# Optimization experiments

Hardware: AMD Instinct MI355X
Metric: run time of the kernel (lower is better)

## Reference

```python
import jax, jax.numpy as jnp
import numpy as np

D = 768  # inputdim = k_size = v_size (forced equal by residual + LayerNorm)
B, T = 16, 2048


def setup_inputs() -> dict:
    key = jax.random.key(0)
    ks = jax.random.split(key, 9)
    s = 1.0 / np.sqrt(D)
    return {
        "x": jax.random.normal(ks[0], (B, T, D), dtype=jnp.float32),
        "Wk": jax.random.normal(ks[1], (D, D), dtype=jnp.float32) * s,
        "bk": jnp.zeros((D,), dtype=jnp.float32),
        "Wq": jax.random.normal(ks[2], (D, D), dtype=jnp.float32) * s,
        "bq": jnp.zeros((D,), dtype=jnp.float32),
        "Wv": jax.random.normal(ks[3], (D, D), dtype=jnp.float32) * s,
        "bv": jnp.zeros((D,), dtype=jnp.float32),
        "gamma": jnp.ones((D,), dtype=jnp.float32),
        "beta": jnp.zeros((D,), dtype=jnp.float32),
    }


def reference(x, Wk, bk, Wq, bq, Wv, bv, gamma, beta):
    sq_k = jnp.sqrt(jnp.asarray(D, dtype=x.dtype))
    keys = jnp.einsum("btd,kd->btk", x, Wk) + bk      # [B,T,K]
    queries = jnp.einsum("btd,kd->btk", x, Wq) + bq   # [B,T,K]
    values = jnp.einsum("btd,vd->btv", x, Wv) + bv    # [B,T,V]
    logits = jnp.einsum("bqk,btk->bqt", queries, keys)  # [B,Tq,Tk]
    # NB: original softmaxes over dim=1 (the QUERY axis), then scales AFTER softmax
    q_k = jax.nn.softmax(logits, axis=1) / sq_k
    applied = jnp.einsum("bqt,btv->bqv", q_k, values)  # [B,T,V]
    y = applied + x
    mu = jnp.mean(y, axis=-1, keepdims=True)
    var = jnp.mean(jnp.square(y - mu), axis=-1, keepdims=True)
    return (y - mu) * jax.lax.rsqrt(var + 1e-5) * gamma + beta
```

## Files before the change

kernel.cpp:

```cpp
#include <hip/hip_runtime.h>
#include <hip/hip_fp16.h>

#define DD 768
#define BB 16
#define TT 2048
#define BT (BB*TT)
#define NQS 8
#define BST 76

using f16 = _Float16;
typedef __attribute__((ext_vector_type(8))) f16 half8;
typedef __attribute__((ext_vector_type(4))) f16 half4;
typedef __attribute__((ext_vector_type(4))) float f32x4;

#define GSWZ(r) ((((r) & 3)) ^ (((r) >> 2) & 3))

typedef const __attribute__((address_space(1))) unsigned int* gas1;
typedef __attribute__((address_space(3))) unsigned int* las3;
__device__ __forceinline__ void gload16(const void* g, void* l){
  __builtin_amdgcn_global_load_lds((gas1)g, (las3)l, 16, 0, 0);
}

__global__ __launch_bounds__(256)
void tofp16_kernel(const float* __restrict__ src, f16* __restrict__ dst, int n4){
  const int stride = gridDim.x * 256;
  for (int i = blockIdx.x*256 + threadIdx.x; i < n4; i += stride){
    float4 v = ((const float4*)src)[i];
    half4 h; h[0]=(f16)v.x; h[1]=(f16)v.y; h[2]=(f16)v.z; h[3]=(f16)v.w;
    ((half4*)dst)[i] = h;
  }
}

template<int OMODE>
__global__ __launch_bounds__(256, OMODE==2 ? 3 : 2)
void gemmk(const f16* __restrict__ A, int lda, long sA,
           const f16* __restrict__ B, int ldb, long sB,
           void* __restrict__ Out, int ldc, long sC,
           const float* __restrict__ aux, int Kdim,
           float* __restrict__ f0, float* __restrict__ f1,
           const f16* __restrict__ cs, f16* __restrict__ vt)
{
  constexpr int MR = (OMODE==2) ? 4 : 8;
  constexpr int BM = MR * 32;
  constexpr int AC = BM / 64;

  __shared__ f16 lA[3][BM*32];
  __shared__ f16 lB[3][128*32];
  __shared__ float smx[OMODE==1 ? 4 : 1][4][16], szx[OMODE==1 ? 4 : 1][4][16];
  __shared__ f16 lCC[OMODE==2 ? 2048 : 8];

  const int nx = gridDim.x, ny = gridDim.y, nwg = nx * ny, cpx = nwg >> 3;
  int h = blockIdx.x + nx * blockIdx.y;
  h = (h & 7) * cpx + (h >> 3);
  const int bx = h / ny, by = h % ny;

  const int b = blockIdx.z;
  const f16* A_ = A + (size_t)b * sA;
  const f16* B_ = B + (size_t)b * sB;
  const int m0 = bx * BM, n0 = by * 128;
  const int tid = threadIdx.x, lane = tid & 63, wave = tid >> 6;
  const int wm = wave >> 1, wn = wave & 1;

  size_t gaO[AC], gbO[2];
#pragma unroll
  for (int k = 0; k < AC; ++k){
    int c = k*256 + tid, r = c >> 2, s = (c & 3) ^ GSWZ(r);
    gaO[k] = (size_t)(m0 + r) * lda + s * 8;
  }
#pragma unroll
  for (int k = 0; k < 2; ++k){
    int c = k*256 + tid, r = c >> 2, s = (c & 3) ^ GSWZ(r);
    gbO[k] = (size_t)(n0 + r) * ldb + s * 8;
  }

  f32x4 acc[MR][4] = {};
  const int NT = Kdim >> 5;

  auto STAGE = [&](int u, int kt){
#pragma unroll
    for (int k = 0; k < AC; ++k) gload16(A_ + gaO[k] + kt, &lA[u][(k*256+tid)*8]);
#pragma unroll
    for (int k = 0; k < 2; ++k)  gload16(B_ + gbO[k] + kt, &lB[u][(k*256+tid)*8]);
  };

  if constexpr (OMODE == 2){
    const f16* cb = cs + ((size_t)b * NQS + (bx >> 1)) * TT;
    ((half8*)lCC)[tid] = ((const half8*)cb)[tid];
    __syncthreads();
  }

  STAGE(0, 0); STAGE(1, 32);

  const int frow = lane & 15;
  const int rsl = (((lane >> 4) ^ GSWZ(frow)) & 3) * 8;
  const int tsl = (lane >> 4) * 8;
  const int offA = (wm*(MR*16) + frow)*32 + rsl;
  const int offB = (wn*64 + frow)*32 + rsl;

  int u = 0;
  for (int t = 0; t < NT; ++t){
    int u2 = u + 2; if (u2 >= 3) u2 -= 3;
    __builtin_amdgcn_s_barrier();
    __builtin_amdgcn_sched_barrier(0);
    if (t + 2 < NT) STAGE(u2, (t + 2) * 32);
    const int rem = NT - 1 - t;
    if constexpr (AC == 4){
      if (rem >= 2)      asm volatile("s_waitcnt vmcnt(12)" ::: "memory");
      else if (rem == 1) asm volatile("s_waitcnt vmcnt(6)"  ::: "memory");
      else               asm volatile("s_waitcnt vmcnt(0)"  ::: "memory");
    } else {
      if (rem >= 2)      asm volatile("s_waitcnt vmcnt(8)" ::: "memory");
      else if (rem == 1) asm volatile("s_waitcnt vmcnt(4)" ::: "memory");
      else               asm volatile("s_waitcnt vmcnt(0)" ::: "memory");
    }
    __builtin_amdgcn_s_barrier();
    __builtin_amdgcn_sched_barrier(0);

    const f16* tA = &lA[u][0] + offA;
    const f16* tB = &lB[u][0] + offB;
    half8 af[MR], bf[4];
#pragma unroll
    for (int i = 0; i < MR; ++i) af[i] = *(const half8*)(tA + i*512);
#pragma unroll
    for (int j = 0; j < 4; ++j)  bf[j] = *(const half8*)(tB + j*512);
    if constexpr (OMODE == 2){
      half8 cc = *(const half8*)&lCC[t*32 + tsl];
#pragma unroll
      for (int i = 0; i < MR; ++i) af[i] *= cc;
    }
    __builtin_amdgcn_s_setprio(1);
#pragma unroll
    for (int i = 0; i < MR; ++i)
#pragma unroll
      for (int j = 0; j < 4; ++j)
        acc[i][j] = __builtin_amdgcn_mfma_f32_16x16x32_f16(af[i], bf[j], acc[i][j], 0,0,0);
    __builtin_amdgcn_s_setprio(0);
    u = (u + 1 == 3) ? 0 : u + 1;
  }

  __syncthreads();
  const int kq4 = (lane >> 4) * 4;
  f16* bnc = &lA[0][0] + wave * (16*BST);
  const int rrow = lane >> 2, rcol = (lane & 3) * 16;

  if constexpr (OMODE == 0 || OMODE == 2){
    const bool toVt = (OMODE == 0) && (b == 2);
    float bias4[4] = {};
    if constexpr (OMODE == 0){
#pragma unroll
      for (int j = 0; j < 4; ++j) bias4[j] = aux[b*DD + n0 + wn*64 + j*16 + frow];
    }
    f16* O = (OMODE == 0) ? ((f16*)Out + (size_t)b * sC) : ((f16*)Out + (size_t)b * sC);
#pragma unroll
    for (int i = 0; i < MR; ++i){
#pragma unroll
      for (int j = 0; j < 4; ++j)
#pragma unroll
        for (int r = 0; r < 4; ++r)
          bnc[(kq4 + r)*BST + j*16 + frow] = (f16)(acc[i][j][r] + bias4[j]);
      if (!toVt){
        half8 w0 = *(const half8*)&bnc[rrow*BST + rcol];
        half8 w1 = *(const half8*)&bnc[rrow*BST + rcol + 8];
        const int gr = m0 + wm*(MR*16) + i*16 + rrow;
        const int gc = n0 + wn*64 + rcol;
        *(half8*)&O[(size_t)gr*ldc + gc]     = w0;
        *(half8*)&O[(size_t)gr*ldc + gc + 8] = w1;
      } else {
        f16 tmp[16];
#pragma unroll
        for (int k = 0; k < 16; ++k) tmp[k] = bnc[k*BST + lane];
        half8 v0, v1;
#pragma unroll
        for (int k = 0; k < 8; ++k){ v0[k] = tmp[k]; v1[k] = tmp[8+k]; }
        const int tokg = m0 + wm*(MR*16) + i*16;
        const int batch = tokg >> 11, tok = tokg & (TT-1);
        f16* Vo = vt + ((size_t)batch*DD + n0 + wn*64 + lane)*TT + tok;
        *(half8*)&Vo[0] = v0;
        *(half8*)&Vo[8] = v1;
      }
    }
  } else {
    f16* O = (f16*)Out + (size_t)b * sC;
    float Mb[4];
#pragma unroll
    for (int j = 0; j < 4; ++j){
      float mx = acc[0][j][0];
#pragma unroll
      for (int i = 0; i < MR; ++i)
#pragma unroll
        for (int r = 0; r < 4; ++r) mx = fmaxf(mx, acc[i][j][r]);
      mx = fmaxf(mx, __shfl_xor(mx, 16, 64));
      mx = fmaxf(mx, __shfl_xor(mx, 32, 64));
      if (lane < 16) smx[wave][j][lane] = mx;
      Mb[j] = mx;
    }
    __syncthreads();
#pragma unroll
    for (int j = 0; j < 4; ++j)
      Mb[j] = fmaxf(Mb[j], smx[wave ^ 2][j][frow]);
    float zz[4] = {};
#pragma unroll
    for (int i = 0; i < MR; ++i){
#pragma unroll
      for (int j = 0; j < 4; ++j)
#pragma unroll
        for (int r = 0; r < 4; ++r){
          float e = __expf(acc[i][j][r] - Mb[j]);
          zz[j] += e;
          bnc[(kq4 + r)*BST + j*16 + frow] = (f16)e;
        }
      half8 w0 = *(const half8*)&bnc[rrow*BST + rcol];
      half8 w1 = *(const half8*)&bnc[rrow*BST + rcol + 8];
      const int gr = m0 + wm*(MR*16) + i*16 + rrow;
      const int gc = n0 + wn*64 + rcol;
      *(half8*)&O[(size_t)gr*ldc + gc]     = w0;
      *(half8*)&O[(size_t)gr*ldc + gc + 8] = w1;
    }
#pragma unroll
    for (int j = 0; j < 4; ++j){
      zz[j] += __shfl_xor(zz[j], 16, 64);
      zz[j] += __shfl_xor(zz[j], 32, 64);
      if (lane < 16) szx[wave][j][lane] = zz[j];
    }
    __syncthreads();
    if (wm == 0 && lane < 16){
#pragma unroll
      for (int j = 0; j < 4; ++j){
        const int gc = n0 + wn*64 + j*16 + lane;
        size_t o = ((size_t)b * NQS + bx) * TT + gc;
        f0[o] = Mb[j];
        f1[o] = zz[j] + szx[wave + 2][j][lane];
      }
    }
  }
}

__global__ __launch_bounds__(256)
void statsB_kernel(const float* __restrict__ pm, const float* __restrict__ pz,
                   f16* __restrict__ c){
  const int b = blockIdx.y;
  const int t = blockIdx.x * 256 + threadIdx.x;
  float am[NQS], az[NQS];
#pragma unroll
  for (int k = 0; k < NQS; ++k){
    size_t o = ((size_t)b * NQS + k) * TT + t;
    am[k] = pm[o]; az[k] = pz[o];
  }
  float M = am[0];
#pragma unroll
  for (int k = 1; k < NQS; ++k) M = fmaxf(M, am[k]);
  float Z = 0.f;
#pragma unroll
  for (int k = 0; k < NQS; ++k) Z += az[k] * __expf(am[k] - M);
  const float zi = 1.f / (Z * 27.712812921102035f);
#pragma unroll
  for (int k = 0; k < NQS; ++k)
    c[((size_t)b * NQS + k) * TT + t] = (f16)(__expf(am[k] - M) * zi);
}

__global__ __launch_bounds__(192)
void ln2_kernel(const half4* __restrict__ applied, const float4* __restrict__ x,
                const float4* __restrict__ gamma4, const float4* __restrict__ beta4,
                float4* __restrict__ out){
  const size_t base = (size_t)blockIdx.x * (DD/4);
  const int cc = threadIdx.x;
  half4 a4 = applied[base + cc];
  float4 x4 = x[base + cc];
  float y0 = (float)a4[0] + x4.x;
  float y1 = (float)a4[1] + x4.y;
  float y2 = (float)a4[2] + x4.z;
  float y3 = (float)a4[3] + x4.w;
  float s = y0+y1+y2+y3;
  float sq = y0*y0+y1*y1+y2*y2+y3*y3;
#pragma unroll
  for (int off = 32; off > 0; off >>= 1){
    s  += __shfl_down(s,  off, 64);
    sq += __shfl_down(sq, off, 64);
  }
  __shared__ float rs_[3], rq_[3];
  const int lane = threadIdx.x & 63, w = threadIdx.x >> 6;
  if (lane == 0){ rs_[w] = s; rq_[w] = sq; }
  __syncthreads();
  const float S_ = rs_[0]+rs_[1]+rs_[2];
  const float Q_ = rq_[0]+rq_[1]+rq_[2];
  const float mu  = S_ * (1.f/DD);
  const float var = Q_ * (1.f/DD) - mu*mu;
  const float rstd = rsqrtf(var + 1e-5f);
  float4 g = gamma4[cc], be = beta4[cc], o;
  o.x = (y0 - mu)*rstd*g.x + be.x;
  o.y = (y1 - mu)*rstd*g.y + be.y;
  o.z = (y2 - mu)*rstd*g.z + be.z;
  o.w = (y3 - mu)*rstd*g.w + be.w;
  out[base + cc] = o;
}

extern "C" void kernel_launch(void* const* d_in, const int* in_sizes, int n_in,
                              void* d_out, int out_size, void* d_ws, size_t ws_size,
                              hipStream_t stream)
{
  const float* x    = (const float*)d_in[0];
  const float* Wk   = (const float*)d_in[1];
  const float* bk   = (const float*)d_in[2];
  const float* Wq   = (const float*)d_in[3];
  const float* bq   = (const float*)d_in[4];
  const float* Wv   = (const float*)d_in[5];
  const float* bv   = (const float*)d_in[6];
  const float* gamma= (const float*)d_in[7];
  const float* beta = (const float*)d_in[8];
  float* out = (float*)d_out;

  const size_t PW = (size_t)DD*DD*2;
  const size_t PB = (size_t)TT*DD*2;
  const size_t T4 = (size_t)TT*4;
  auto al = [](size_t n){ return (n + 255) & ~(size_t)255; };

  auto need = [&](int G)->size_t{
    size_t t = al(3*PW) + al(3*DD*4) + al((size_t)BB*PB) + al((size_t)BB*TT*TT*2)
             + al((size_t)G*PB) + al(2*(size_t)G*PB)
             + 2*al((size_t)G*NQS*T4) + al((size_t)BB*NQS*TT*2);
    if (3*(size_t)G*PB < (size_t)BB*PB) t += al((size_t)BB*PB);
    return t;
  };

  int G = 0;
  for (int g : {16, 8, 4, 2, 1}) if (need(g) <= ws_size){ G = g; break; }
  if (G == 0) return;

  char* p = (char*)d_ws;
  auto alloc = [&](size_t n)->char*{ char* r = p; p += (n + 255) & ~(size_t)255; return r; };
  f16*   Wf    = (f16*)alloc(3*PW);
  float* biasf = (float*)alloc(3*DD*4);
  f16*   Vt    = (f16*)alloc((size_t)BB*PB);
  f16*   P16   = (f16*)alloc((size_t)BB*TT*TT*2);
  f16*   Xc    = (f16*)alloc((size_t)G*PB);
  f16*   QKVc  = (f16*)alloc(2*(size_t)G*PB);
  float* pm    = (float*)alloc((size_t)G*NQS*T4);
  float* pz    = (float*)alloc((size_t)G*NQS*T4);
  f16*   cbuf  = (f16*)alloc((size_t)BB*NQS*TT*2);
  f16* applied = (3*(size_t)G*PB >= (size_t)BB*PB) ? Xc
               : (f16*)alloc((size_t)BB*PB);
  f16* Qc = QKVc, *Kc = QKVc + (size_t)G*TT*DD;

  tofp16_kernel<<<288, 256, 0, stream>>>(Wq, Wf,             DD*DD/4);
  tofp16_kernel<<<288, 256, 0, stream>>>(Wk, Wf +   DD*DD,   DD*DD/4);
  tofp16_kernel<<<288, 256, 0, stream>>>(Wv, Wf + 2*DD*DD,   DD*DD/4);
  hipMemcpyAsync(biasf,        bq, DD*4, hipMemcpyDeviceToDevice, stream);
  hipMemcpyAsync(biasf +   DD, bk, DD*4, hipMemcpyDeviceToDevice, stream);
  hipMemcpyAsync(biasf + 2*DD, bv, DD*4, hipMemcpyDeviceToDevice, stream);

  const int nRows = G * TT;
  for (int b0 = 0; b0 < BB; b0 += G){
    tofp16_kernel<<<2048, 256, 0, stream>>>(x + (size_t)b0*TT*DD, Xc, nRows*DD/4);

    dim3 gp(nRows/256, DD/128, 3);
    gemmk<0><<<gp, 256, 0, stream>>>(Xc, DD, 0, Wf, DD, (long)DD*DD,
                                     QKVc, DD, (long)G*TT*DD, biasf, DD,
                                     nullptr, nullptr, nullptr,
                                     Vt + (size_t)b0*DD*TT);

    dim3 gs(TT/256, TT/128, G);
    gemmk<1><<<gs, 256, 0, stream>>>(Qc, DD, (long)TT*DD, Kc, DD, (long)TT*DD,
                                     P16 + (size_t)b0*TT*TT, TT, (long)TT*TT,
                                     nullptr, DD, pm, pz, nullptr, nullptr);

    statsB_kernel<<<dim3(TT/256, G), 256, 0, stream>>>(
        pm, pz, cbuf + (size_t)b0*NQS*TT);
  }

  dim3 gpv(TT/128, DD/128, BB);
  gemmk<2><<<gpv, 256, 0, stream>>>(P16, TT, (long)TT*TT, Vt, TT, (long)DD*TT,
                                    applied, DD, (long)TT*DD, nullptr, TT,
                                    nullptr, nullptr, cbuf, nullptr);

  ln2_kernel<<<BT, 192, 0, stream>>>((const half4*)applied, (const float4*)x,
                                     (const float4*)gamma, (const float4*)beta,
                                     (float4*)out);
}
```

Before: 538.8 us.

## Replace QK^T logits GEMM with 256x256-tile 8-wave kernel with explicit pipelining

Adds a dedicated gemm8p kernel for the Q·K^T logits plus exp/column-stats epilogue. It uses 512 threads, 256x256 output tiles and double-buffered LDS stages, with hand-scheduled waitcnt and barrier phases interleaving async global-to-LDS loads with MFMA groups. The goal is more operand reuse per tile and better overlap of loads with math than the generic 256x128 gemmk<1>. The softmax epilogue is removed from gemmk, which now serves only the projection and PV modes. The cost is one workgroup per CU with large LDS use, and the fragile manual vmcnt accounting must stay correct.

```diff
diff --git a/kernel.cpp b/kernel.cpp
--- a/kernel.cpp
+++ b/kernel.cpp
@@ -31,13 +31,161 @@
   }
 }
 
+__global__ __launch_bounds__(512, 1)
+void gemm8p(const f16* __restrict__ Q, const f16* __restrict__ K,
+            f16* __restrict__ P, float* __restrict__ pm, float* __restrict__ pz)
+{
+  __shared__ f16 bufA[2][2][256*32];
+  __shared__ f16 bufB[2][2][256*32];
+  __shared__ float smx[8][4][16], szx[8][4][16];
+
+  int h = blockIdx.x + 8 * blockIdx.y;
+  h = (h & 7) * 8 + (h >> 3);
+  const int bx = h >> 3, by = h & 7;
+
+  const int b = blockIdx.z;
+  const f16* Qb = Q + (size_t)b * TT * DD;
+  const f16* Kb = K + (size_t)b * TT * DD;
+  f16* O = P + (size_t)b * TT * TT;
+  const int m0 = bx * 256, n0 = by * 256;
+  const int tid = threadIdx.x, lane = tid & 63, wave = tid >> 6;
+  const int wm = wave >> 2, wn = wave & 3;
+
+  const int c0 = tid, c1 = 512 + tid;
+  const int r0 = c0 >> 2, s0c = (c0 & 3) ^ GSWZ(r0);
+  const int r1 = c1 >> 2, s1c = (c1 & 3) ^ GSWZ(r1);
+  const size_t ga0 = (size_t)(m0 + r0) * DD + s0c * 8;
+  const size_t ga1 = (size_t)(m0 + r1) * DD + s1c * 8;
+  const size_t gb0 = (size_t)(n0 + r0) * DD + s0c * 8;
+  const size_t gb1 = (size_t)(n0 + r1) * DD + s1c * 8;
+
+#define STGA(PAR, S, TILE) do{ f16* _d = &bufA[PAR][S][0]; \
+    const int _k = (TILE)*64 + (S)*32; \
+    gload16(Qb + ga0 + _k, _d + c0*8); gload16(Qb + ga1 + _k, _d + c1*8); }while(0)
+#define STGB(PAR, S, TILE) do{ f16* _d = &bufB[PAR][S][0]; \
+    const int _k = (TILE)*64 + (S)*32; \
+    gload16(Kb + gb0 + _k, _d + c0*8); gload16(Kb + gb1 + _k, _d + c1*8); }while(0)
+#define VMW(N) asm volatile("s_waitcnt vmcnt(" #N ")" ::: "memory")
+
+  f32x4 acc[8][4] = {};
+
+  const int frow = lane & 15;
+  const int rsl = (((lane >> 4) ^ GSWZ(frow)) & 3) * 8;
+  const int offA = (wm*128 + frow)*32 + rsl;
+  const int offB = (wn*64 + frow)*32 + rsl;
+
+  STGA(0,0,0); STGB(0,0,0); STGA(0,1,0); STGB(0,1,0); STGA(1,0,1); STGB(1,0,1);
+  VMW(8);
+  __builtin_amdgcn_s_barrier();
+  __builtin_amdgcn_sched_barrier(0);
+
+#define MM(MRH, II, JJ) acc[(MRH)*4+(II)][JJ] = \
+    __builtin_amdgcn_mfma_f32_16x16x32_f16(af##II, bf##JJ, acc[(MRH)*4+(II)][JJ], 0,0,0)
+#define PHASE(MRH, S, PAR, STAGE_STMT, CKPT_STMT) do{ \
+    const f16* _a = &bufA[PAR][S][0] + offA + (MRH)*2048; \
+    const f16* _b = &bufB[PAR][S][0] + offB; \
+    half8 af0 = *(const half8*)(_a); \
+    half8 af1 = *(const half8*)(_a + 512); \
+    half8 af2 = *(const half8*)(_a + 1024); \
+    half8 af3 = *(const half8*)(_a + 1536); \
+    half8 bf0 = *(const half8*)(_b); \
+    half8 bf1 = *(const half8*)(_b + 512); \
+    half8 bf2 = *(const half8*)(_b + 1024); \
+    half8 bf3 = *(const half8*)(_b + 1536); \
+    STAGE_STMT; \
+    CKPT_STMT; \
+    asm volatile("s_waitcnt lgkmcnt(0)" ::: "memory"); \
+    __builtin_amdgcn_sched_barrier(0); \
+    __builtin_amdgcn_s_setprio(1); \
+    MM(MRH,0,0); MM(MRH,0,1); MM(MRH,0,2); MM(MRH,0,3); \
+    MM(MRH,1,0); MM(MRH,1,1); MM(MRH,1,2); MM(MRH,1,3); \
+    MM(MRH,2,0); MM(MRH,2,1); MM(MRH,2,2); MM(MRH,2,3); \
+    MM(MRH,3,0); MM(MRH,3,1); MM(MRH,3,2); MM(MRH,3,3); \
+    __builtin_amdgcn_s_setprio(0); \
+    __builtin_amdgcn_s_barrier(); \
+    __builtin_amdgcn_sched_barrier(0); \
+  }while(0)
+
+  for (int i = 0; i < 6; ++i){
+    const bool lastI = (i == 5);
+    PHASE(0, 0, 0, STGA(1,1, 2*i+1), );
+    PHASE(1, 0, 0, STGB(1,1, 2*i+1), VMW(8));
+    PHASE(0, 1, 0, if(!lastI) STGA(0,0, 2*i+2), );
+    PHASE(1, 1, 0, if(!lastI) STGB(0,0, 2*i+2), if(!lastI) VMW(8); else VMW(4));
+    PHASE(0, 0, 1, if(!lastI) STGA(0,1, 2*i+2), );
+    PHASE(1, 0, 1, if(!lastI) STGB(0,1, 2*i+2), if(!lastI) VMW(8); else VMW(0));
+    PHASE(0, 1, 1, if(!lastI) STGA(1,0, 2*i+3), );
+    PHASE(1, 1, 1, if(!lastI) STGB(1,0, 2*i+3), if(!lastI) VMW(8));
+  }
+#undef PHASE
+#undef MM
+#undef STGA
+#undef STGB
+#undef VMW
+
+  const int kq4 = (lane >> 4) * 4;
+  f16* bnc = &bufA[0][0][0] + wave * (16*BST);
+  const int rrow = lane >> 2, rcol = (lane & 3) * 16;
+
+  float Mb[4];
+#pragma unroll
+  for (int j = 0; j < 4; ++j){
+    float mx = acc[0][j][0];
+#pragma unroll
+    for (int i = 0; i < 8; ++i)
+#pragma unroll
+      for (int r = 0; r < 4; ++r) mx = fmaxf(mx, acc[i][j][r]);
+    mx = fmaxf(mx, __shfl_xor(mx, 16, 64));
+    mx = fmaxf(mx, __shfl_xor(mx, 32, 64));
+    if (lane < 16) smx[wave][j][lane] = mx;
+    Mb[j] = mx;
+  }
+  __syncthreads();
+#pragma unroll
+  for (int j = 0; j < 4; ++j)
+    Mb[j] = fmaxf(Mb[j], smx[wave ^ 4][j][frow]);
+  float zz[4] = {};
+#pragma unroll
+  for (int i = 0; i < 8; ++i){
+#pragma unroll
+    for (int j = 0; j < 4; ++j)
+#pragma unroll
+      for (int r = 0; r < 4; ++r){
+        float e = __expf(acc[i][j][r] - Mb[j]);
+        zz[j] += e;
+        bnc[(kq4 + r)*BST + j*16 + frow] = (f16)e;
+      }
+    half8 w0 = *(const half8*)&bnc[rrow*BST + rcol];
+    half8 w1 = *(const half8*)&bnc[rrow*BST + rcol + 8];
+    const int gr = m0 + wm*128 + i*16 + rrow;
+    const int gc = n0 + wn*64 + rcol;
+    *(half8*)&O[(size_t)gr*TT + gc]     = w0;
+    *(half8*)&O[(size_t)gr*TT + gc + 8] = w1;
+  }
+#pragma unroll
+  for (int j = 0; j < 4; ++j){
+    zz[j] += __shfl_xor(zz[j], 16, 64);
+    zz[j] += __shfl_xor(zz[j], 32, 64);
+    if (lane < 16) szx[wave][j][lane] = zz[j];
+  }
+  __syncthreads();
+  if (wm == 0 && lane < 16){
+#pragma unroll
+    for (int j = 0; j < 4; ++j){
+      const int gc = n0 + wn*64 + j*16 + lane;
+      size_t o = ((size_t)b * NQS + bx) * TT + gc;
+      pm[o] = Mb[j];
+      pz[o] = zz[j] + szx[wave + 4][j][lane];
+    }
+  }
+}
+
 template<int OMODE>
 __global__ __launch_bounds__(256, OMODE==2 ? 3 : 2)
 void gemmk(const f16* __restrict__ A, int lda, long sA,
            const f16* __restrict__ B, int ldb, long sB,
            void* __restrict__ Out, int ldc, long sC,
            const float* __restrict__ aux, int Kdim,
-           float* __restrict__ f0, float* __restrict__ f1,
            const f16* __restrict__ cs, f16* __restrict__ vt)
 {
   constexpr int MR = (OMODE==2) ? 4 : 8;
@@ -46,7 +194,6 @@
 
   __shared__ f16 lA[3][BM*32];
   __shared__ f16 lB[3][128*32];
-  __shared__ float smx[OMODE==1 ? 4 : 1][4][16], szx[OMODE==1 ? 4 : 1][4][16];
   __shared__ f16 lCC[OMODE==2 ? 2048 : 8];
 
   const int nx = gridDim.x, ny = gridDim.y, nwg = nx * ny, cpx = nwg >> 3;
@@ -143,94 +290,39 @@
   f16* bnc = &lA[0][0] + wave * (16*BST);
   const int rrow = lane >> 2, rcol = (lane & 3) * 16;
 
-  if constexpr (OMODE == 0 || OMODE == 2){
-    const bool toVt = (OMODE == 0) && (b == 2);
-    float bias4[4] = {};
-    if constexpr (OMODE == 0){
-#pragma unroll
-      for (int j = 0; j < 4; ++j) bias4[j] = aux[b*DD + n0 + wn*64 + j*16 + frow];
-    }
-    f16* O = (OMODE == 0) ? ((f16*)Out + (size_t)b * sC) : ((f16*)Out + (size_t)b * sC);
-#pragma unroll
-    for (int i = 0; i < MR; ++i){
-#pragma unroll
-      for (int j = 0; j < 4; ++j)
-#pragma unroll
-        for (int r = 0; r < 4; ++r)
-          bnc[(kq4 + r)*BST + j*16 + frow] = (f16)(acc[i][j][r] + bias4[j]);
-      if (!toVt){
-        half8 w0 = *(const half8*)&bnc[rrow*BST + rcol];
-        half8 w1 = *(const half8*)&bnc[rrow*BST + rcol + 8];
-        const int gr = m0 + wm*(MR*16) + i*16 + rrow;
-        const int gc = n0 + wn*64 + rcol;
-        *(half8*)&O[(size_t)gr*ldc + gc]     = w0;
-        *(half8*)&O[(size_t)gr*ldc + gc + 8] = w1;
-      } else {
-        f16 tmp[16];
-#pragma unroll
-        for (int k = 0; k < 16; ++k) tmp[k] = bnc[k*BST + lane];
-        half8 v0, v1;
-#pragma unroll
-        for (int k = 0; k < 8; ++k){ v0[k] = tmp[k]; v1[k] = tmp[8+k]; }
-        const int tokg = m0 + wm*(MR*16) + i*16;
-        const int batch = tokg >> 11, tok = tokg & (TT-1);
-        f16* Vo = vt + ((size_t)batch*DD + n0 + wn*64 + lane)*TT + tok;
-        *(half8*)&Vo[0] = v0;
-        *(half8*)&Vo[8] = v1;
-      }
-    }
-  } else {
-    f16* O = (f16*)Out + (size_t)b * sC;
-    float Mb[4];
-#pragma unroll
-    for (int j = 0; j < 4; ++j){
-      float mx = acc[0][j][0];
-#pragma unroll
-      for (int i = 0; i < MR; ++i)
-#pragma unroll
-        for (int r = 0; r < 4; ++r) mx = fmaxf(mx, acc[i][j][r]);
-      mx = fmaxf(mx, __shfl_xor(mx, 16, 64));
-      mx = fmaxf(mx, __shfl_xor(mx, 32, 64));
-      if (lane < 16) smx[wave][j][lane] = mx;
-      Mb[j] = mx;
-    }
-    __syncthreads();
+  const bool toVt = (OMODE == 0) && (b == 2);
+  float bias4[4] = {};
+  if constexpr (OMODE == 0){
+#pragma unroll
+    for (int j = 0; j < 4; ++j) bias4[j] = aux[b*DD + n0 + wn*64 + j*16 + frow];
+  }
+  f16* O = (f16*)Out + (size_t)b * sC;
+#pragma unroll
+  for (int i = 0; i < MR; ++i){
 #pragma unroll
     for (int j = 0; j < 4; ++j)
-      Mb[j] = fmaxf(Mb[j], smx[wave ^ 2][j][frow]);
-    float zz[4] = {};
-#pragma unroll
-    for (int i = 0; i < MR; ++i){
-#pragma unroll
-      for (int j = 0; j < 4; ++j)
-#pragma unroll
-        for (int r = 0; r < 4; ++r){
-          float e = __expf(acc[i][j][r] - Mb[j]);
-          zz[j] += e;
-          bnc[(kq4 + r)*BST + j*16 + frow] = (f16)e;
-        }
+#pragma unroll
+      for (int r = 0; r < 4; ++r)
+        bnc[(kq4 + r)*BST + j*16 + frow] = (f16)(acc[i][j][r] + bias4[j]);
+    if (!toVt){
       half8 w0 = *(const half8*)&bnc[rrow*BST + rcol];
       half8 w1 = *(const half8*)&bnc[rrow*BST + rcol + 8];
       const int gr = m0 + wm*(MR*16) + i*16 + rrow;
       const int gc = n0 + wn*64 + rcol;
       *(half8*)&O[(size_t)gr*ldc + gc]     = w0;
       *(half8*)&O[(size_t)gr*ldc + gc + 8] = w1;
-    }
-#pragma unroll
-    for (int j = 0; j < 4; ++j){
-      zz[j] += __shfl_xor(zz[j], 16, 64);
-      zz[j] += __shfl_xor(zz[j], 32, 64);
-      if (lane < 16) szx[wave][j][lane] = zz[j];
-    }
-    __syncthreads();
-    if (wm == 0 && lane < 16){
-#pragma unroll
-      for (int j = 0; j < 4; ++j){
-        const int gc = n0 + wn*64 + j*16 + lane;
-        size_t o = ((size_t)b * NQS + bx) * TT + gc;
-        f0[o] = Mb[j];
-        f1[o] = zz[j] + szx[wave + 2][j][lane];
-      }
+    } else {
+      f16 tmp[16];
+#pragma unroll
+      for (int k = 0; k < 16; ++k) tmp[k] = bnc[k*BST + lane];
+      half8 v0, v1;
+#pragma unroll
+      for (int k = 0; k < 8; ++k){ v0[k] = tmp[k]; v1[k] = tmp[8+k]; }
+      const int tokg = m0 + wm*(MR*16) + i*16;
+      const int batch = tokg >> 11, tok = tokg & (TT-1);
+      f16* Vo = vt + ((size_t)batch*DD + n0 + wn*64 + lane)*TT + tok;
+      *(half8*)&Vo[0] = v0;
+      *(half8*)&Vo[8] = v1;
     }
   }
 }
@@ -355,13 +447,10 @@
     dim3 gp(nRows/256, DD/128, 3);
     gemmk<0><<<gp, 256, 0, stream>>>(Xc, DD, 0, Wf, DD, (long)DD*DD,
                                      QKVc, DD, (long)G*TT*DD, biasf, DD,
-                                     nullptr, nullptr, nullptr,
-                                     Vt + (size_t)b0*DD*TT);
-
-    dim3 gs(TT/256, TT/128, G);
-    gemmk<1><<<gs, 256, 0, stream>>>(Qc, DD, (long)TT*DD, Kc, DD, (long)TT*DD,
-                                     P16 + (size_t)b0*TT*TT, TT, (long)TT*TT,
-                                     nullptr, DD, pm, pz, nullptr, nullptr);
+                                     nullptr, Vt + (size_t)b0*DD*TT);
+
+    dim3 gs(8, 8, G);
+    gemm8p<<<gs, 512, 0, stream>>>(Qc, Kc, P16 + (size_t)b0*TT*TT, pm, pz);
 
     statsB_kernel<<<dim3(TT/256, G), 256, 0, stream>>>(
         pm, pz, cbuf + (size_t)b0*NQS*TT);
@@ -370,7 +459,7 @@
   dim3 gpv(TT/128, DD/128, BB);
   gemmk<2><<<gpv, 256, 0, stream>>>(P16, TT, (long)TT*TT, Vt, TT, (long)DD*TT,
                                     applied, DD, (long)TT*DD, nullptr, TT,
-                                    nullptr, nullptr, cbuf, nullptr);
+                                    cbuf, nullptr);
 
   ln2_kernel<<<BT, 192, 0, stream>>>((const half4*)applied, (const float4*)x,
                                      (const float4*)gamma, (const float4*)beta,
```

After: 540.3 us. About the same (+0.3%).
